# Kernel optimization log

Measured on AMD Instinct MI355X. Metric: run time of the kernel, lower is better.

The kernel has to match this reference:

```python
import jax, jax.numpy as jnp
import numpy as np

B, M, H, D, K, V = 32, 4096, 32, 4096, 128, 128

def setup_inputs() -> dict:
    key = jax.random.key(0)
    ks = jax.random.split(key, 7)
    s = lambda fan: 1.0 / np.sqrt(fan)
    return {
        "x": jax.random.normal(ks[0], (B, D), jnp.float32),
        "K_prev": jax.random.normal(ks[1], (B, M, K), jnp.float32),
        "V_prev": jax.random.normal(ks[2], (B, M, V), jnp.float32),
        "P_q": jax.random.normal(ks[3], (H, D, K), jnp.float32) * s(D),
        "P_k": jax.random.normal(ks[4], (D, K), jnp.float32) * s(D),
        "P_v": jax.random.normal(ks[5], (D, V), jnp.float32) * s(D),
        "P_o": jax.random.normal(ks[6], (H, D, V), jnp.float32) * s(D),
    }

def reference(x, K_prev, V_prev, P_q, P_k, P_v, P_o):
    # per-head query projection: [b,d] x [h,d,k] -> [b,h,k]
    q = jnp.einsum('bd,hdk->bhk', x, P_q)
    # shared (multi-query) K/V projection of the new token, appended to cache
    k_new = jnp.einsum('bd,dk->bk', x, P_k)          # [b,k]
    v_new = jnp.einsum('bd,dv->bv', x, P_v)          # [b,v]
    K_new = jnp.concatenate([K_prev, k_new[:, None, :]], axis=1)  # [b,m+1,k]
    V_new = jnp.concatenate([V_prev, v_new[:, None, :]], axis=1)  # [b,m+1,v]
    # attention over shared cache
    logits = jnp.einsum('bhk,bmk->bhm', q, K_new)    # [b,h,m+1]
    w = jax.nn.softmax(logits, axis=-1)
    o = jnp.einsum('bhm,bmv->bhv', w, V_new)         # [b,h,v]
    y = jnp.einsum('bhv,hdv->bd', o, P_o)            # [b,d]
    return (y, K_new, V_new)
```

## Files before the change

kernel.cpp:

```cpp
#include <hip/hip_runtime.h>

#define B_ 32
#define M_ 4096
#define M1_ 4097
#define H_ 32
#define D_ 4096

typedef float float4_ __attribute__((ext_vector_type(4)));
typedef float f32x4 __attribute__((ext_vector_type(4)));
typedef short short8 __attribute__((ext_vector_type(8)));
typedef short short4_ __attribute__((ext_vector_type(4)));

#define KOFF 131072
#define VOFF 16912384

#define Q_OFF     0u
#define O_OFF     139264u
#define YPART_OFF 270336u
#define QPART_OFF 1318912u
#define APO_OFF   1318912u
#define MSUM_OFF  5513216u

__device__ __forceinline__ unsigned short f2bf(float f) {
  union { float f; unsigned u; } cv; cv.f = f;
  return (unsigned short)((cv.u + 0x7FFFu + ((cv.u >> 16) & 1u)) >> 16);
}
__device__ __forceinline__ float bf2f(unsigned short b) {
  union { unsigned u; float f; } cv; cv.u = ((unsigned)b) << 16;
  return cv.f;
}
__device__ __forceinline__ short8 pack8(const float* t) {
  short8 r;
#pragma unroll
  for (int j = 0; j < 8; ++j) r[j] = (short)f2bf(t[j]);
  return r;
}
__device__ __forceinline__ short8 load8cvt(const float* __restrict__ p) {
  float t[8];
  float4_ v0 = *(const float4_*)p;
  float4_ v1 = *(const float4_*)(p + 4);
#pragma unroll
  for (int j = 0; j < 4; ++j) { t[j] = v0[j]; t[4 + j] = v1[j]; }
  return pack8(t);
}

__global__ __launch_bounds__(256, 4) void k_proj(const float* __restrict__ x,
    const float* __restrict__ Pq, const float* __restrict__ Pk,
    const float* __restrict__ Pv, float* __restrict__ qpart)
{
  __shared__ unsigned short Wl[2][32][128];
  int bid = blockIdx.x;
  int hh = bid >> 4;
  int c  = bid & 15;
  const float* W = (hh < 32) ? (Pq + (size_t)hh * D_ * 128)
                             : ((hh == 32) ? Pk : Pv);
  int d0 = c * 256;
  int tid = threadIdx.x;
  int w = tid >> 6, l = tid & 63, l15 = l & 15, lg = l >> 4;
  f32x4 acc[2][2] = {};
  for (int ks = 0; ks < 8; ++ks) {
    int buf = ks & 1;
#pragma unroll
    for (int i = 0; i < 4; ++i) {
      int idx = i * 256 + tid;
      int dr = idx >> 5, k4 = (idx & 31) * 4;
      float4_ t = *(const float4_*)(W + (size_t)(d0 + ks * 32 + dr) * 128 + k4);
      short4_ s;
#pragma unroll
      for (int j = 0; j < 4; ++j) s[j] = (short)f2bf(t[j]);
      *(short4_*)&Wl[buf][dr][k4] = s;
    }
    __syncthreads();
    int dk = d0 + ks * 32 + lg * 8;
    short8 af[2];
#pragma unroll
    for (int bt = 0; bt < 2; ++bt)
      af[bt] = load8cvt(x + (size_t)(bt * 16 + l15) * D_ + dk);
    short8 bf[2];
#pragma unroll
    for (int nti = 0; nti < 2; ++nti) {
      int col = (2 * w + nti) * 16 + l15;
      short8 t;
#pragma unroll
      for (int j = 0; j < 8; ++j) t[j] = (short)Wl[buf][lg * 8 + j][col];
      bf[nti] = t;
    }
#pragma unroll
    for (int bt = 0; bt < 2; ++bt)
#pragma unroll
      for (int nti = 0; nti < 2; ++nti)
        acc[bt][nti] = __builtin_amdgcn_mfma_f32_16x16x32_bf16(af[bt], bf[nti], acc[bt][nti], 0, 0, 0);
  }
#pragma unroll
  for (int bt = 0; bt < 2; ++bt)
#pragma unroll
    for (int nti = 0; nti < 2; ++nti) {
      int k = (2 * w + nti) * 16 + l15;
#pragma unroll
      for (int i = 0; i < 4; ++i) {
        int b = bt * 16 + lg * 4 + i;
        qpart[(size_t)((c * 34 + hh) * 32 + b) * 128 + k] = acc[bt][nti][i];
      }
    }
}

__global__ __launch_bounds__(256) void k_reduce_q(const float* __restrict__ qpart,
    float* __restrict__ q, float* __restrict__ dout)
{
  int idx = blockIdx.x * 256 + threadIdx.x;
  if (idx >= 34 * 32 * 128) return;
  float s = 0.f;
#pragma unroll
  for (int cc = 0; cc < 16; ++cc) s += qpart[(size_t)cc * 139264 + idx];
  q[idx] = s;
  int hh = idx >> 12;
  if (hh >= 32) {
    int b = (idx >> 7) & 31, k = idx & 127;
    size_t off = (hh == 32) ? (size_t)KOFF : (size_t)VOFF;
    dout[off + ((size_t)b * M1_ + M_) * 128 + k] = s;
  }
}

__global__ __launch_bounds__(256, 4) void k_attn(const float* __restrict__ Kp,
    const float* __restrict__ Vp, const float* __restrict__ q,
    float* __restrict__ dout, unsigned short* __restrict__ apo,
    float* __restrict__ msum)
{
  __shared__ unsigned short Vl[64][128];
  __shared__ float S[32][73];
  __shared__ unsigned short P[32][64];
  __shared__ float smax[32], ssum[32], sextra[32];
  int bid = blockIdx.x;
  int b = bid >> 6, c = bid & 63;
  int m0 = c * 64;
  int tid = threadIdx.x, w = tid >> 6, l = tid & 63, l15 = l & 15, lg = l >> 4;
  const float* Kt = Kp + ((size_t)b * M_ + m0) * 128;
  const float* Vt = Vp + ((size_t)b * M_ + m0) * 128;
  float* Kn = dout + KOFF + ((size_t)b * M1_ + m0) * 128;
  float* Vn = dout + VOFF + ((size_t)b * M1_ + m0) * 128;

  float4_ kr[8], vr[8];
#pragma unroll
  for (int i = 0; i < 8; ++i) kr[i] = ((const float4_*)Kt)[tid + i * 256];
#pragma unroll
  for (int i = 0; i < 8; ++i) vr[i] = ((const float4_*)Vt)[tid + i * 256];
#pragma unroll
  for (int i = 0; i < 8; ++i) ((float4_*)Kn)[tid + i * 256] = kr[i];
#pragma unroll
  for (int i = 0; i < 8; ++i) {
    int idx = tid + i * 256;
    ((float4_*)Vn)[idx] = vr[i];
    int m = idx >> 5, v = (idx & 31) * 4;
    short4_ s;
#pragma unroll
    for (int j = 0; j < 4; ++j) s[j] = (short)f2bf(vr[i][j]);
    *(short4_*)&Vl[m][v] = s;
  }

  f32x4 sacc[2] = {};
#pragma unroll
  for (int ks = 0; ks < 4; ++ks) {
    short8 bfK = load8cvt(Kt + (size_t)(w * 16 + l15) * 128 + ks * 32 + lg * 8);
#pragma unroll
    for (int ht = 0; ht < 2; ++ht) {
      short8 af = load8cvt(q + (size_t)((ht * 16 + l15) * 32 + b) * 128 + ks * 32 + lg * 8);
      sacc[ht] = __builtin_amdgcn_mfma_f32_16x16x32_bf16(af, bfK, sacc[ht], 0, 0, 0);
    }
  }
#pragma unroll
  for (int ht = 0; ht < 2; ++ht)
#pragma unroll
    for (int i = 0; i < 4; ++i)
      S[ht * 16 + lg * 4 + i][w * 16 + l15] = sacc[ht][i];

  if (c == 63 && tid < 32) {
    int h = tid;
    const float* qh = q + (size_t)(h * 32 + b) * 128;
    const float* kn = q + (size_t)(32 * 32 + b) * 128;
    float s = 0.f;
    for (int k = 0; k < 128; ++k) s += qh[k] * kn[k];
    S[h][64] = s;
  }
  __syncthreads();

  {
    int h = tid >> 3, i = tid & 7;
    float vals[8];
    float mx = -3e38f;
#pragma unroll
    for (int j = 0; j < 8; ++j) { vals[j] = S[h][i * 8 + j]; mx = fmaxf(mx, vals[j]); }
#pragma unroll
    for (int d = 1; d < 8; d <<= 1) mx = fmaxf(mx, __shfl_xor(mx, d));
    if (c == 63) mx = fmaxf(mx, S[h][64]);
    float se = 0.f;
    short8 pw;
#pragma unroll
    for (int j = 0; j < 8; ++j) {
      float p = __expf(vals[j] - mx);
      se += p;
      pw[j] = (short)f2bf(p);
    }
    *(short8*)((char*)P + h * 128 + ((i * 16) ^ ((h & 7) << 4))) = pw;
    if (c == 63 && i == 0) { float pe = __expf(S[h][64] - mx); se += pe; sextra[h] = pe; }
#pragma unroll
    for (int d = 1; d < 8; d <<= 1) se += __shfl_xor(se, d);
    if (i == 0) { smax[h] = mx; ssum[h] = se; }
  }
  __syncthreads();

  f32x4 oacc[2][2] = {};
#pragma unroll
  for (int ksv = 0; ksv < 2; ++ksv) {
    short8 af[2];
#pragma unroll
    for (int ht = 0; ht < 2; ++ht) {
      int h = ht * 16 + l15;
      af[ht] = *(const short8*)((const char*)P + h * 128 + ((ksv * 64 + lg * 16) ^ ((h & 7) << 4)));
    }
    short8 bf[2];
#pragma unroll
    for (int vti = 0; vti < 2; ++vti) {
      int v = w * 32 + vti * 16 + l15;
      short8 t;
#pragma unroll
      for (int j = 0; j < 8; ++j) t[j] = (short)Vl[ksv * 32 + lg * 8 + j][v];
      bf[vti] = t;
    }
#pragma unroll
    for (int ht = 0; ht < 2; ++ht)
#pragma unroll
      for (int vti = 0; vti < 2; ++vti)
        oacc[ht][vti] = __builtin_amdgcn_mfma_f32_16x16x32_bf16(af[ht], bf[vti], oacc[ht][vti], 0, 0, 0);
  }

  const float* vnew = q + (size_t)(33 * 32 + b) * 128;
#pragma unroll
  for (int ht = 0; ht < 2; ++ht)
#pragma unroll
    for (int vti = 0; vti < 2; ++vti) {
      int v = w * 32 + vti * 16 + l15;
#pragma unroll
      for (int i = 0; i < 4; ++i) {
        int h = ht * 16 + lg * 4 + i;
        float val = oacc[ht][vti][i];
        if (c == 63) val += sextra[h] * vnew[v];
        apo[((size_t)(b * 64 + c) * 32 + h) * 128 + v] = f2bf(val);
      }
    }
  if (tid < 32) {
    size_t base = ((size_t)(b * 64 + c) * 32 + tid) * 2;
    msum[base]     = smax[tid];
    msum[base + 1] = ssum[tid];
  }
}

__global__ void k_combine(const unsigned short* __restrict__ apo,
    const float* __restrict__ msum, float* __restrict__ o)
{
  int bid = blockIdx.x;
  int b = bid >> 5, h = bid & 31;
  int v = threadIdx.x;
  float gm = -3e38f;
  for (int cc = 0; cc < 64; ++cc)
    gm = fmaxf(gm, msum[((size_t)(b * 64 + cc) * 32 + h) * 2]);
  float num = 0.f, den = 0.f;
  for (int cc = 0; cc < 64; ++cc) {
    size_t slot = (size_t)(b * 64 + cc) * 32 + h;
    float sc = __expf(msum[slot * 2] - gm);
    num += sc * bf2f(apo[slot * 128 + v]);
    den += sc * msum[slot * 2 + 1];
  }
  o[((size_t)(b * 32 + h)) * 128 + v] = num / den;
}

__global__ __launch_bounds__(256) void k_out(const float* __restrict__ o,
    const float* __restrict__ Po, float* __restrict__ ypart)
{
  int bid = blockIdx.x;
  int dt = bid >> 3, hg = bid & 7;
  int tid = threadIdx.x, w = tid >> 6, l = tid & 63, l15 = l & 15, lg = l >> 4;
  f32x4 acc[2][2] = {};
  for (int hi = 0; hi < 4; ++hi) {
    int h = hg * 4 + hi;
#pragma unroll
    for (int ks = 0; ks < 4; ++ks) {
      short8 af[2], bf[2];
#pragma unroll
      for (int bt = 0; bt < 2; ++bt)
        af[bt] = load8cvt(o + ((size_t)((bt * 16 + l15) * 32 + h)) * 128 + ks * 32 + lg * 8);
#pragma unroll
      for (int dtl = 0; dtl < 2; ++dtl) {
        int d = dt * 128 + (2 * w + dtl) * 16 + l15;
        bf[dtl] = load8cvt(Po + ((size_t)h * D_ + d) * 128 + ks * 32 + lg * 8);
      }
#pragma unroll
      for (int bt = 0; bt < 2; ++bt)
#pragma unroll
        for (int dtl = 0; dtl < 2; ++dtl)
          acc[bt][dtl] = __builtin_amdgcn_mfma_f32_16x16x32_bf16(af[bt], bf[dtl], acc[bt][dtl], 0, 0, 0);
    }
  }
#pragma unroll
  for (int bt = 0; bt < 2; ++bt)
#pragma unroll
    for (int dtl = 0; dtl < 2; ++dtl) {
      int d = dt * 128 + (2 * w + dtl) * 16 + l15;
#pragma unroll
      for (int i = 0; i < 4; ++i) {
        int b = bt * 16 + lg * 4 + i;
        ypart[((size_t)(hg * 32 + b)) * 4096 + d] = acc[bt][dtl][i];
      }
    }
}

__global__ __launch_bounds__(256) void k_reduce_y(const float* __restrict__ ypart,
    float* __restrict__ dout)
{
  int idx = blockIdx.x * 256 + threadIdx.x;
  float s = 0.f;
#pragma unroll
  for (int g = 0; g < 8; ++g) s += ypart[(size_t)g * 131072 + idx];
  dout[idx] = s;
}

extern "C" void kernel_launch(void* const* d_in, const int* in_sizes, int n_in,
                              void* d_out, int out_size, void* d_ws, size_t ws_size,
                              hipStream_t stream) {
  (void)in_sizes; (void)n_in; (void)out_size; (void)ws_size;
  const float* x  = (const float*)d_in[0];
  const float* Kp = (const float*)d_in[1];
  const float* Vp = (const float*)d_in[2];
  const float* Pq = (const float*)d_in[3];
  const float* Pk = (const float*)d_in[4];
  const float* Pv = (const float*)d_in[5];
  const float* Po = (const float*)d_in[6];
  float* out = (float*)d_out;
  float* ws  = (float*)d_ws;
  float* q     = ws + Q_OFF;
  float* o     = ws + O_OFF;
  float* ypart = ws + YPART_OFF;
  float* qpart = ws + QPART_OFF;
  unsigned short* apo = (unsigned short*)(ws + APO_OFF);
  float* msum  = ws + MSUM_OFF;

  hipLaunchKernelGGL(k_proj,     dim3(544),  dim3(256), 0, stream, x, Pq, Pk, Pv, qpart);
  hipLaunchKernelGGL(k_reduce_q, dim3(544),  dim3(256), 0, stream, qpart, q, out);
  hipLaunchKernelGGL(k_attn,     dim3(2048), dim3(256), 0, stream, Kp, Vp, q, out, apo, msum);
  hipLaunchKernelGGL(k_combine,  dim3(1024), dim3(128), 0, stream, apo, msum, o);
  hipLaunchKernelGGL(k_out,      dim3(256),  dim3(256), 0, stream, o, Po, ypart);
  hipLaunchKernelGGL(k_reduce_y, dim3(512),  dim3(256), 0, stream, ypart, out);
}
```

Baseline: 149.6 us.

## Double grid sizes for projection and output GEMMs, prefetch weight tiles into registers

The Q/K/V projection kernel splits D into 32 chunks of 128 instead of 16 of 256, doubling its block count, and register-prefetches the next weight tile while the current one is converted to bf16 in LDS. The q reduction now sums 32 partials, and the workspace offset for msum moves to make room for the larger partial buffer. The output projection halves each block's d-tile to 64 columns, launching twice as many blocks. A sched_barrier is added in the attention kernel so all K/V loads are issued before the stores. The goal is better occupancy on the weight-bandwidth-bound GEMMs, at the cost of more partial-sum traffic and reduction work.

```diff
diff --git a/kernel.cpp b/kernel.cpp
--- a/kernel.cpp
+++ b/kernel.cpp
@@ -19,7 +19,7 @@
 #define YPART_OFF 270336u
 #define QPART_OFF 1318912u
 #define APO_OFF   1318912u
-#define MSUM_OFF  5513216u
+#define MSUM_OFF  5775360u
 
 __device__ __forceinline__ unsigned short f2bf(float f) {
   union { float f; unsigned u; } cv; cv.f = f;
@@ -50,25 +50,32 @@
 {
   __shared__ unsigned short Wl[2][32][128];
   int bid = blockIdx.x;
-  int hh = bid >> 4;
-  int c  = bid & 15;
+  int hh = bid >> 5;
+  int c  = bid & 31;
   const float* W = (hh < 32) ? (Pq + (size_t)hh * D_ * 128)
                              : ((hh == 32) ? Pk : Pv);
-  int d0 = c * 256;
+  int d0 = c * 128;
   int tid = threadIdx.x;
   int w = tid >> 6, l = tid & 63, l15 = l & 15, lg = l >> 4;
+  int sdr = tid >> 5, sk4 = (tid & 31) * 4;
   f32x4 acc[2][2] = {};
-  for (int ks = 0; ks < 8; ++ks) {
+  float4_ tmp[4];
+#pragma unroll
+  for (int i = 0; i < 4; ++i)
+    tmp[i] = *(const float4_*)(W + (size_t)(d0 + (i * 8 + sdr)) * 128 + sk4);
+  for (int ks = 0; ks < 4; ++ks) {
     int buf = ks & 1;
 #pragma unroll
     for (int i = 0; i < 4; ++i) {
-      int idx = i * 256 + tid;
-      int dr = idx >> 5, k4 = (idx & 31) * 4;
-      float4_ t = *(const float4_*)(W + (size_t)(d0 + ks * 32 + dr) * 128 + k4);
       short4_ s;
 #pragma unroll
-      for (int j = 0; j < 4; ++j) s[j] = (short)f2bf(t[j]);
-      *(short4_*)&Wl[buf][dr][k4] = s;
+      for (int j = 0; j < 4; ++j) s[j] = (short)f2bf(tmp[i][j]);
+      *(short4_*)&Wl[buf][i * 8 + sdr][sk4] = s;
+    }
+    if (ks < 3) {
+#pragma unroll
+      for (int i = 0; i < 4; ++i)
+        tmp[i] = *(const float4_*)(W + (size_t)(d0 + (ks + 1) * 32 + i * 8 + sdr) * 128 + sk4);
     }
     __syncthreads();
     int dk = d0 + ks * 32 + lg * 8;
@@ -111,7 +118,7 @@
   if (idx >= 34 * 32 * 128) return;
   float s = 0.f;
 #pragma unroll
-  for (int cc = 0; cc < 16; ++cc) s += qpart[(size_t)cc * 139264 + idx];
+  for (int cc = 0; cc < 32; ++cc) s += qpart[(size_t)cc * 139264 + idx];
   q[idx] = s;
   int hh = idx >> 12;
   if (hh >= 32) {
@@ -144,6 +151,7 @@
   for (int i = 0; i < 8; ++i) kr[i] = ((const float4_*)Kt)[tid + i * 256];
 #pragma unroll
   for (int i = 0; i < 8; ++i) vr[i] = ((const float4_*)Vt)[tid + i * 256];
+  __builtin_amdgcn_sched_barrier(0);
 #pragma unroll
   for (int i = 0; i < 8; ++i) ((float4_*)Kn)[tid + i * 256] = kr[i];
 #pragma unroll
@@ -279,37 +287,28 @@
   int bid = blockIdx.x;
   int dt = bid >> 3, hg = bid & 7;
   int tid = threadIdx.x, w = tid >> 6, l = tid & 63, l15 = l & 15, lg = l >> 4;
-  f32x4 acc[2][2] = {};
+  int d = dt * 64 + w * 16 + l15;
+  f32x4 acc[2] = {};
   for (int hi = 0; hi < 4; ++hi) {
     int h = hg * 4 + hi;
 #pragma unroll
     for (int ks = 0; ks < 4; ++ks) {
-      short8 af[2], bf[2];
+      short8 af[2];
 #pragma unroll
       for (int bt = 0; bt < 2; ++bt)
         af[bt] = load8cvt(o + ((size_t)((bt * 16 + l15) * 32 + h)) * 128 + ks * 32 + lg * 8);
-#pragma unroll
-      for (int dtl = 0; dtl < 2; ++dtl) {
-        int d = dt * 128 + (2 * w + dtl) * 16 + l15;
-        bf[dtl] = load8cvt(Po + ((size_t)h * D_ + d) * 128 + ks * 32 + lg * 8);
-      }
+      short8 bf = load8cvt(Po + ((size_t)h * D_ + d) * 128 + ks * 32 + lg * 8);
 #pragma unroll
       for (int bt = 0; bt < 2; ++bt)
-#pragma unroll
-        for (int dtl = 0; dtl < 2; ++dtl)
-          acc[bt][dtl] = __builtin_amdgcn_mfma_f32_16x16x32_bf16(af[bt], bf[dtl], acc[bt][dtl], 0, 0, 0);
+        acc[bt] = __builtin_amdgcn_mfma_f32_16x16x32_bf16(af[bt], bf, acc[bt], 0, 0, 0);
     }
   }
 #pragma unroll
   for (int bt = 0; bt < 2; ++bt)
 #pragma unroll
-    for (int dtl = 0; dtl < 2; ++dtl) {
-      int d = dt * 128 + (2 * w + dtl) * 16 + l15;
-#pragma unroll
-      for (int i = 0; i < 4; ++i) {
-        int b = bt * 16 + lg * 4 + i;
-        ypart[((size_t)(hg * 32 + b)) * 4096 + d] = acc[bt][dtl][i];
-      }
+    for (int i = 0; i < 4; ++i) {
+      int b = bt * 16 + lg * 4 + i;
+      ypart[((size_t)(hg * 32 + b)) * 4096 + d] = acc[bt][i];
     }
 }
 
@@ -343,10 +342,10 @@
   unsigned short* apo = (unsigned short*)(ws + APO_OFF);
   float* msum  = ws + MSUM_OFF;
 
-  hipLaunchKernelGGL(k_proj,     dim3(544),  dim3(256), 0, stream, x, Pq, Pk, Pv, qpart);
+  hipLaunchKernelGGL(k_proj,     dim3(1088), dim3(256), 0, stream, x, Pq, Pk, Pv, qpart);
   hipLaunchKernelGGL(k_reduce_q, dim3(544),  dim3(256), 0, stream, qpart, q, out);
   hipLaunchKernelGGL(k_attn,     dim3(2048), dim3(256), 0, stream, Kp, Vp, q, out, apo, msum);
   hipLaunchKernelGGL(k_combine,  dim3(1024), dim3(128), 0, stream, apo, msum, o);
-  hipLaunchKernelGGL(k_out,      dim3(256),  dim3(256), 0, stream, o, Po, ypart);
+  hipLaunchKernelGGL(k_out,      dim3(512),  dim3(256), 0, stream, o, Po, ypart);
   hipLaunchKernelGGL(k_reduce_y, dim3(512),  dim3(256), 0, stream, ypart, out);
 }
```

New measurement: 152.3 us. Within noise of the previous version (+1.8%).
